# Kernel tuning notes

Hardware: AMD Instinct MI355X
Metric: run time of the kernel (lower is better)

## Reference

```python
import jax, jax.numpy as jnp
import numpy as np

NEG_SLOPE = 0.2

def _leaky(x):
    return jnp.where(x >= 0, x, NEG_SLOPE * x)

def _unigat(X, W, b, ae, av, pair_e, pair_v, num_v, num_e):
    # theta
    Xp = X @ W + b                                                    # [N, d]
    # v2e mean aggregation -> hyperedge features
    deg_e = jax.ops.segment_sum(jnp.ones(pair_e.shape, jnp.float32), pair_e, num_segments=num_e)
    Y = jax.ops.segment_sum(Xp[pair_v], pair_e, num_segments=num_e) / jnp.maximum(deg_e, 1.0)[:, None]  # [E, d]
    # GAT-style attention per incidence pair (edge term + node term), dropout=identity in eval
    s = _leaky((Y @ ae)[pair_e] + (Xp @ av)[pair_v])                  # [P]
    # segment softmax over edges incident to each node
    m = jax.ops.segment_max(s, pair_v, num_segments=num_v)
    ex = jnp.exp(s - m[pair_v])
    den = jax.ops.segment_sum(ex, pair_v, num_segments=num_v)
    alpha = ex / den[pair_v]                                          # [P]
    out = jax.ops.segment_sum(alpha[:, None] * Y[pair_e], pair_v, num_segments=num_v)  # [N, d]
    return jax.nn.elu(out)  # is_last=False everywhere -> ELU (use_bn=False)

def _multi_head(X, W, b, ae, av, pair_e, pair_v, num_v, num_e):
    # W:[H,din,d] b:[H,d] ae/av:[H,d]; concat heads on feature dim
    f = lambda Wh, bh, aeh, avh: _unigat(X, Wh, bh, aeh, avh, pair_e, pair_v, num_v, num_e)
    outs = jax.vmap(f)(W, b, ae, av)                                  # [H, N, d]
    return jnp.transpose(outs, (1, 0, 2)).reshape(X.shape[0], -1)     # [N, H*d]

def setup_inputs() -> dict:
    key = jax.random.key(0)
    ks = jax.random.split(key, 12)
    N, E, P = 100000, 20000, 1600000
    din, dh, H, C = 128, 64, 4, 40
    concat = 2
    inp = {
        "x0": jax.random.normal(ks[0], (N, din), jnp.float32),
        "x1": jax.random.normal(ks[1], (N, din), jnp.float32),
        "W1": jax.random.normal(ks[2], (H, din, dh), jnp.float32) * 0.05,
        "b1": jnp.zeros((H, dh), jnp.float32),
        "ae1": jax.random.normal(ks[3], (H, dh), jnp.float32) * 0.05,
        "av1": jax.random.normal(ks[4], (H, dh), jnp.float32) * 0.05,
        "W2": jax.random.normal(ks[5], (concat * dh * H, C), jnp.float32) * 0.05,
        "b2": jnp.zeros((C,), jnp.float32),
        "ae2": jax.random.normal(ks[6], (C,), jnp.float32) * 0.05,
        "av2": jax.random.normal(ks[7], (C,), jnp.float32) * 0.05,
        "pair_e": jax.random.randint(ks[8], (P,), 0, E, jnp.int32),
        "pair_v": jax.random.randint(ks[9], (P,), 0, N, jnp.int32),
        "num_v": N,
        "num_e": E,
    }
    return inp

def reference(x0, x1, W1, b1, ae1, av1, W2, b2, ae2, av2, pair_e, pair_v, num_v, num_e):
    # dropout layers are identity in eval mode
    h0 = _multi_head(x0, W1, b1, ae1, av1, pair_e, pair_v, num_v, num_e)
    h1 = _multi_head(x1, W1, b1, ae1, av1, pair_e, pair_v, num_v, num_e)
    h = jnp.concatenate([h0, h1], axis=-1)                            # [N, concat*H*dh]
    return _unigat(h, W2, b2, ae2, av2, pair_e, pair_v, num_v, num_e) # [N, C]
```

## Files before the change

kernel.cpp:

```cpp
#include <hip/hip_runtime.h>
#include <cstdint>
#include <cstddef>

static constexpr int DIN = 128;
static constexpr int DH = 64;
static constexpr int NH = 4;
static constexpr int DCAT = 512;
static constexpr int NC = 40;
static constexpr int E_CONST = 20000;
static constexpr int SH_V = 9, SUBD_V = 512;
static constexpr int SH_E = 7, SUBD_E = 128;
static constexpr int ECH = 11, NSUB_E = 10;
static constexpr int VCH = 12, NSUB_V = 25;
static constexpr int CHUNKA = 4096;

typedef unsigned short u16;
typedef __attribute__((ext_vector_type(4))) unsigned short u16x4;
typedef __attribute__((ext_vector_type(8))) unsigned short u16x8;
typedef __attribute__((ext_vector_type(8))) short bf16x8;
typedef __attribute__((ext_vector_type(4))) float f32x4;

static __device__ __forceinline__ float bf2f(u16 u) {
    union { unsigned int i; float f; } x;
    x.i = ((unsigned int)u) << 16;
    return x.f;
}
static __device__ __forceinline__ u16 f2bf(float f) {
    union { float f; unsigned int i; } x;
    x.f = f;
    unsigned int r = x.i + 0x7fffu + ((x.i >> 16) & 1u);
    return (u16)(r >> 16);
}


__global__ void k_hist2(const int* __restrict__ pv, const int* __restrict__ pe,
                        int* __restrict__ btot_v, int* __restrict__ btot_e, int P) {
    __shared__ int cv[256], ce[256];
    int tid = threadIdx.x;
    cv[tid] = 0; ce[tid] = 0;
    __syncthreads();
    int p0 = blockIdx.x * CHUNKA;
    #pragma unroll
    for (int j = 0; j < CHUNKA / 256; ++j) {
        int p = p0 + tid + j * 256;
        if (p < P) {
            atomicAdd(&cv[pv[p] >> SH_V], 1);
            atomicAdd(&ce[pe[p] >> SH_E], 1);
        }
    }
    __syncthreads();
    if (cv[tid]) atomicAdd(&btot_v[tid], cv[tid]);
    if (ce[tid]) atomicAdd(&btot_e[tid], ce[tid]);
}

__global__ void k_scan_small(int* __restrict__ a, int n) {
    __shared__ int wsum[16];
    __shared__ int carry_s;
    int tid = threadIdx.x;
    int lane = tid & 63;
    int w = tid >> 6;
    if (tid == 0) carry_s = 0;
    __syncthreads();
    for (int base = 0; base < n; base += 1024) {
        int i = base + tid;
        int v = (i < n) ? a[i] : 0;
        int x = v;
        #pragma unroll
        for (int off = 1; off < 64; off <<= 1) {
            int t = __shfl_up(x, off);
            if (lane >= off) x += t;
        }
        if (lane == 63) wsum[w] = x;
        __syncthreads();
        int woff = 0;
        for (int k = 0; k < w; ++k) woff += wsum[k];
        int carry = carry_s;
        if (i < n) a[i] = carry + woff + x - v;
        int tot = 0;
        for (int k = 0; k < 16; ++k) tot += wsum[k];
        __syncthreads();
        if (tid == 0) carry_s = carry + tot;
        __syncthreads();
    }
    if (tid == 0) a[n] = carry_s;
}

__global__ void k_scatter2way(const int* __restrict__ pv, const int* __restrict__ pe,
                              const int* __restrict__ bstart_v, const int* __restrict__ bstart_e,
                              int* __restrict__ cur_v, int* __restrict__ cur_e,
                              uint2* __restrict__ sorted_v, uint2* __restrict__ sorted_e, int P) {
    __shared__ int cv[256], ce[256], posv[256], pose[256];
    int tid = threadIdx.x;
    cv[tid] = 0; ce[tid] = 0;
    __syncthreads();
    int p0 = blockIdx.x * CHUNKA;
    int kv[CHUNKA / 256], ke[CHUNKA / 256];
    #pragma unroll
    for (int j = 0; j < CHUNKA / 256; ++j) {
        int p = p0 + tid + j * 256;
        if (p < P) {
            kv[j] = pv[p];
            ke[j] = pe[p];
            atomicAdd(&cv[kv[j] >> SH_V], 1);
            atomicAdd(&ce[ke[j] >> SH_E], 1);
        } else {
            kv[j] = -1;
            ke[j] = -1;
        }
    }
    __syncthreads();
    if (cv[tid]) posv[tid] = bstart_v[tid] + atomicAdd(&cur_v[tid], cv[tid]);
    if (ce[tid]) pose[tid] = bstart_e[tid] + atomicAdd(&cur_e[tid], ce[tid]);
    __syncthreads();
    #pragma unroll
    for (int j = 0; j < CHUNKA / 256; ++j) {
        if (kv[j] >= 0) {
            int iv = atomicAdd(&posv[kv[j] >> SH_V], 1);
            sorted_v[iv] = make_uint2((unsigned)kv[j], (unsigned)ke[j]);
            int ie = atomicAdd(&pose[ke[j] >> SH_E], 1);
            sorted_e[ie] = make_uint2((unsigned)ke[j], (unsigned)kv[j]);
        }
    }
}

template <int SUBD, int SH, int NSUB, int CSH>
__global__ __launch_bounds__(256) void k_build_ord(const uint2* __restrict__ sorted,
                                                   const int* __restrict__ bstart,
                                                   int* __restrict__ start_out,
                                                   int* __restrict__ deg_out,
                                                   int* __restrict__ csr_out, int D) {
    constexpr int NK2 = SUBD * NSUB;
    constexpr int STRIP = (NK2 + 255) / 256;
    __shared__ int cnt[NK2];
    __shared__ int wsum[4];
    int b = blockIdx.x;
    int tid = threadIdx.x;
    int base_key = b << SH;
    int s0 = bstart[b];
    int cntN = bstart[b + 1] - s0;
    for (int k = tid; k < NK2; k += 256) cnt[k] = 0;
    __syncthreads();
    for (int i = tid; i < cntN; i += 256) {
        uint2 pr = sorted[s0 + i];
        int k2 = ((int)pr.x - base_key) * NSUB + ((int)pr.y >> CSH);
        atomicAdd(&cnt[k2], 1);
    }
    __syncthreads();
    int local[STRIP];
    int sum = 0;
    int t0 = tid * STRIP;
    #pragma unroll
    for (int j = 0; j < STRIP; ++j) {
        int idx = t0 + j;
        local[j] = (idx < NK2) ? cnt[idx] : 0;
        sum += local[j];
    }
    int lane = tid & 63, w = tid >> 6;
    int x = sum;
    #pragma unroll
    for (int off = 1; off < 64; off <<= 1) {
        int t = __shfl_up(x, off);
        if (lane >= off) x += t;
    }
    if (lane == 63) wsum[w] = x;
    __syncthreads();
    int woff = 0;
    for (int k = 0; k < w; ++k) woff += wsum[k];
    int run = woff + x - sum;
    __syncthreads();
    #pragma unroll
    for (int j = 0; j < STRIP; ++j) {
        int idx = t0 + j;
        if (idx < NK2) {
            int tmp = local[j];
            cnt[idx] = run;
            run += tmp;
        }
    }
    __syncthreads();
    for (int loc = tid; loc < SUBD; loc += 256) {
        int key = base_key + loc;
        if (key < D) {
            int st = cnt[loc * NSUB];
            int en = (loc == SUBD - 1) ? cntN : cnt[(loc + 1) * NSUB];
            start_out[key] = s0 + st;
            deg_out[key] = en - st;
        }
    }
    __syncthreads();
    for (int i = tid; i < cntN; i += 256) {
        uint2 pr = sorted[s0 + i];
        int k2 = ((int)pr.x - base_key) * NSUB + ((int)pr.y >> CSH);
        int idx = atomicAdd(&cnt[k2], 1);
        csr_out[s0 + idx] = (int)pr.y;
    }
}


__global__ void k_wav(const float* __restrict__ W1, const float* __restrict__ b1,
                      const float* __restrict__ av1, float* __restrict__ wav,
                      float* __restrict__ bav) {
    int h = blockIdx.x;
    int k = threadIdx.x;
    float s = 0.f;
    for (int j = 0; j < DH; ++j) s += W1[(size_t)(h * DIN + k) * DH + j] * av1[h * DH + j];
    wav[h * DIN + k] = s;
    if (k == 0) {
        float t = 0.f;
        for (int j = 0; j < DH; ++j) t += b1[h * DH + j] * av1[h * DH + j];
        bav[h] = t;
    }
}

__global__ void k_build_wcatT(const float* __restrict__ W1, u16* __restrict__ WcatT) {
    int idx = blockIdx.x * 256 + threadIdx.x;
    if (idx >= 256 * DIN) return;
    int c = idx >> 7, k = idx & 127;
    int h = c >> 6, j = c & 63;
    WcatT[c * DIN + k] = f2bf(W1[((size_t)h * DIN + k) * DH + j]);
}

__global__ void k_build_w2T(const float* __restrict__ W2, u16* __restrict__ W2T) {
    int idx = blockIdx.x * 256 + threadIdx.x;
    if (idx >= 48 * DCAT) return;
    int c = idx >> 9, k = idx & 511;
    float v = (c < NC) ? W2[(size_t)k * NC + c] : 0.f;
    W2T[c * DCAT + k] = f2bf(v);
}

__global__ void k_conv(const float* __restrict__ X0, const float* __restrict__ X1,
                       const float* __restrict__ wav, const float* __restrict__ bav,
                       u16* __restrict__ Xbi, float* __restrict__ sv8, int N) {
    int wave = (blockIdx.x * blockDim.x + threadIdx.x) >> 6;
    int lane = threadIdx.x & 63;
    if (wave >= N) return;
    int xz = blockIdx.y;
    const float* X = xz ? X1 : X0;
    float2 a = *(const float2*)(X + (size_t)wave * DIN + lane * 2);
    unsigned int packed = (unsigned int)f2bf(a.x) | ((unsigned int)f2bf(a.y) << 16);
    *(unsigned int*)(Xbi + (size_t)wave * 256 + xz * 128 + lane * 2) = packed;
    float s[NH];
    #pragma unroll
    for (int h = 0; h < NH; ++h) {
        float2 wv = *(const float2*)(wav + h * DIN + lane * 2);
        float t = a.x * wv.x + a.y * wv.y;
        #pragma unroll
        for (int off = 32; off >= 1; off >>= 1) t += __shfl_xor(t, off);
        s[h] = t;
    }
    if (lane == 0) {
        #pragma unroll
        for (int h = 0; h < NH; ++h) sv8[(size_t)wave * 8 + h * 2 + xz] = s[h] + bav[h];
    }
}

__global__ void k_edge_mean1(const u16* __restrict__ Xbi, const int* __restrict__ start_e,
                             const int* __restrict__ deg_e, const int* __restrict__ csr_e_v,
                             u16* __restrict__ Xbar0, u16* __restrict__ Xbar1, int E) {
    int wave = (blockIdx.x * blockDim.x + threadIdx.x) >> 6;
    int lane = threadIdx.x & 63;
    if (wave >= E) return;
    int s = start_e[wave], t = s + deg_e[wave];
    int q = lane >> 4, c = lane & 15;
    float a0[8], a1[8];
    #pragma unroll
    for (int j = 0; j < 8; ++j) { a0[j] = 0.f; a1[j] = 0.f; }
    int i = s + q;
    u16x8 y0A = {0}, y1A = {0}, y0B = {0}, y1B = {0}, y0C = {0}, y1C = {0};
#define EM1_LOAD(Y0, Y1, IDX) { int v_ = csr_e_v[IDX]; \
        const u16* yp_ = Xbi + (size_t)v_ * 256 + c * 8; \
        Y0 = *(const u16x8*)yp_; Y1 = *(const u16x8*)(yp_ + 128); }
#define EM1_CONSUME(Y0, Y1) { \
        _Pragma("unroll") \
        for (int j = 0; j < 8; ++j) { a0[j] += bf2f(Y0[j]); a1[j] += bf2f(Y1[j]); } }
    if (i < t) EM1_LOAD(y0A, y1A, i);
    if (i + 4 < t) EM1_LOAD(y0B, y1B, i + 4);
    if (i + 8 < t) EM1_LOAD(y0C, y1C, i + 8);
    for (; i + 8 < t; i += 12) {
        EM1_CONSUME(y0A, y1A);
        if (i + 12 < t) EM1_LOAD(y0A, y1A, i + 12);
        EM1_CONSUME(y0B, y1B);
        if (i + 16 < t) EM1_LOAD(y0B, y1B, i + 16);
        EM1_CONSUME(y0C, y1C);
        if (i + 20 < t) EM1_LOAD(y0C, y1C, i + 20);
    }
    if (i < t) EM1_CONSUME(y0A, y1A);
    if (i + 4 < t) EM1_CONSUME(y0B, y1B);
#undef EM1_LOAD
#undef EM1_CONSUME
    #pragma unroll
    for (int j = 0; j < 8; ++j) {
        a0[j] += __shfl_xor(a0[j], 16);
        a0[j] += __shfl_xor(a0[j], 32);
        a1[j] += __shfl_xor(a1[j], 16);
        a1[j] += __shfl_xor(a1[j], 32);
    }
    int deg = t - s;
    float inv = 1.f / (float)(deg > 1 ? deg : 1);
    if (q == 0) {
        u16x8 r0, r1;
        #pragma unroll
        for (int j = 0; j < 8; ++j) { r0[j] = f2bf(a0[j] * inv); r1[j] = f2bf(a1[j] * inv); }
        *(u16x8*)(Xbar0 + (size_t)wave * DIN + c * 8) = r0;
        *(u16x8*)(Xbar1 + (size_t)wave * DIN + c * 8) = r1;
    }
}

template <int KDIM, int NTILES, int DOTMODE>
__global__ __launch_bounds__(256) void k_gemm_mfma(const u16* __restrict__ A0,
                                                   const u16* __restrict__ A1, int M,
                                                   const u16* __restrict__ Bt,
                                                   const float* __restrict__ bias,
                                                   u16* __restrict__ out0, u16* __restrict__ out1,
                                                   int ldo, int ncols,
                                                   const float* __restrict__ dvec,
                                                   float* __restrict__ dout) {
    constexpr int LDB = KDIM + 8;
    __shared__ u16 Bs[NTILES * 16 * LDB];
    const u16* A = blockIdx.z ? A1 : A0;
    u16* out = blockIdx.z ? out1 : out0;
    int tid = threadIdx.x;
    int colbase = blockIdx.y * NTILES * 16;
    const u16* Btblk = Bt + (size_t)colbase * KDIM;
    for (int idx = tid * 4; idx < NTILES * 16 * KDIM; idx += 256 * 4) {
        int c = idx / KDIM, k = idx % KDIM;
        *(u16x4*)&Bs[c * LDB + k] = *(const u16x4*)(Btblk + c * KDIM + k);
    }
    __syncthreads();
    int w = tid >> 6, lane = tid & 63;
    int r0 = blockIdx.x * 64 + w * 16;
    int arow = r0 + (lane & 15);
    bool avalid = arow < M;
    const u16* ap = A + (size_t)arow * KDIM + (lane >> 4) * 8;
    f32x4 acc[NTILES];
    #pragma unroll
    for (int nt = 0; nt < NTILES; ++nt) acc[nt] = (f32x4){0.f, 0.f, 0.f, 0.f};
    #pragma unroll
    for (int k0 = 0; k0 < KDIM; k0 += 32) {
        bf16x8 a = (bf16x8)(short)0;
        if (avalid) a = *(const bf16x8*)(ap + k0);
        #pragma unroll
        for (int nt = 0; nt < NTILES; ++nt) {
            bf16x8 b = *(const bf16x8*)&Bs[(nt * 16 + (lane & 15)) * LDB + k0 + (lane >> 4) * 8];
            acc[nt] = __builtin_amdgcn_mfma_f32_16x16x32_bf16(a, b, acc[nt], 0, 0, 0);
        }
    }
    #pragma unroll
    for (int j = 0; j < 4; ++j) {
        int row = r0 + (lane >> 4) * 4 + j;
        float pA = 0.f, pB = 0.f;
        #pragma unroll
        for (int nt = 0; nt < NTILES; ++nt) {
            int col = colbase + nt * 16 + (lane & 15);
            bool cok = col < ncols;
            float val = cok ? acc[nt][j] + bias[col] : 0.f;
            if (DOTMODE == 1) {
                float dv = dvec[col];
                if (nt < NTILES / 2) pA += val * dv; else pB += val * dv;
            } else if (DOTMODE == 2) {
                pA += cok ? val * dvec[col] : 0.f;
            }
            if (row < M && cok) out[(size_t)row * ldo + col] = f2bf(val);
        }
        if (DOTMODE) {
            pA += __shfl_xor(pA, 1);
            pA += __shfl_xor(pA, 2);
            pA += __shfl_xor(pA, 4);
            pA += __shfl_xor(pA, 8);
            if (DOTMODE == 1) {
                pB += __shfl_xor(pB, 1);
                pB += __shfl_xor(pB, 2);
                pB += __shfl_xor(pB, 4);
                pB += __shfl_xor(pB, 8);
            }
            if ((lane & 15) == 0 && row < M) {
                if (DOTMODE == 1) {
                    int hbase = blockIdx.y * 2;
                    int z = blockIdx.z;
                    dout[(size_t)row * 8 + hbase * 2 + z] = pA;
                    dout[(size_t)row * 8 + (hbase + 1) * 2 + z] = pB;
                } else {
                    dout[row] = pA;
                }
            }
        }
    }
}

__global__ void k_node_pass1(const u16* __restrict__ Ycat, const float* __restrict__ se8,
                             const float* __restrict__ sv8, const int* __restrict__ start_v,
                             const int* __restrict__ deg_v, const int* __restrict__ csr_v_e,
                             u16* __restrict__ hbuf, int N) {
    int wave = (blockIdx.x * blockDim.x + threadIdx.x) >> 6;
    int lane = threadIdx.x & 63;
    if (wave >= N) return;
    int p0 = start_v[wave], p1 = p0 + deg_v[wave];
    int g = lane >> 5;
    int c = lane & 31;
    int h = c >> 3;
    u16* orow = hbuf + (size_t)wave * DCAT + c * 8;
    if (p1 == p0) {
        if (g == 0) {
            u16x8 z8 = {0, 0, 0, 0, 0, 0, 0, 0};
            *(u16x8*)orow = z8;
            *(u16x8*)(orow + 256) = z8;
        }
        return;
    }
    float sv0 = sv8[(size_t)wave * 8 + h * 2];
    float sv1 = sv8[(size_t)wave * 8 + h * 2 + 1];
    float den0 = 0.f, den1 = 0.f;
    float a0[8], a1[8];
    #pragma unroll
    for (int j = 0; j < 8; ++j) { a0[j] = 0.f; a1[j] = 0.f; }
    for (int i = p0 + g; i < p1; i += 2) {
        int e = csr_v_e[i];
        float2 s2 = *(const float2*)(se8 + e * 8 + h * 2);
        float x0 = s2.x + sv0;
        float x1 = s2.y + sv1;
        x0 = fmaxf(x0, 0.2f * x0);
        x1 = fmaxf(x1, 0.2f * x1);
        float e0 = __expf(x0);
        float e1 = __expf(x1);
        den0 += e0;
        den1 += e1;
        const u16* yp = Ycat + (size_t)e * 512 + c * 8;
        u16x8 q0 = *(const u16x8*)yp;
        u16x8 q1 = *(const u16x8*)(yp + 256);
        #pragma unroll
        for (int j = 0; j < 8; ++j) { a0[j] += e0 * bf2f(q0[j]); a1[j] += e1 * bf2f(q1[j]); }
    }
    den0 += __shfl_xor(den0, 32);
    den1 += __shfl_xor(den1, 32);
    #pragma unroll
    for (int j = 0; j < 8; ++j) {
        a0[j] += __shfl_xor(a0[j], 32);
        a1[j] += __shfl_xor(a1[j], 32);
    }
    float i0 = 1.f / den0, i1 = 1.f / den1;
    u16x8 r0, r1;
    #pragma unroll
    for (int j = 0; j < 8; ++j) {
        float o0 = a0[j] * i0;
        float o1 = a1[j] * i1;
        o0 = o0 > 0.f ? o0 : __expf(o0) - 1.f;
        o1 = o1 > 0.f ? o1 : __expf(o1) - 1.f;
        r0[j] = f2bf(o0);
        r1[j] = f2bf(o1);
    }
    if (g == 0) {
        *(u16x8*)orow = r0;
        *(u16x8*)(orow + 256) = r1;
    }
}


__global__ void k_edge_mean2(const u16* __restrict__ Xp2b, const int* __restrict__ start_e,
                             const int* __restrict__ deg_ea, const int* __restrict__ csr_e_v,
                             u16* __restrict__ Y2b, const float* __restrict__ ae2,
                             float* __restrict__ se2, int E) {
    int wave = (blockIdx.x * blockDim.x + threadIdx.x) >> 6;
    int lane = threadIdx.x & 63;
    if (wave >= E) return;
    int s = start_e[wave], t = s + deg_ea[wave];
    int g = lane >> 4, c = lane & 15;
    bool act = c < 10;
    float acc[4];
    #pragma unroll
    for (int j = 0; j < 4; ++j) acc[j] = 0.f;
    for (int i = s + g; i < t; i += 4) {
        int v = csr_e_v[i];
        if (act) {
            u16x4 y = *(const u16x4*)(Xp2b + (size_t)v * NC + c * 4);
            acc[0] += bf2f(y.x);
            acc[1] += bf2f(y.y);
            acc[2] += bf2f(y.z);
            acc[3] += bf2f(y.w);
        }
    }
    #pragma unroll
    for (int j = 0; j < 4; ++j) {
        acc[j] += __shfl_xor(acc[j], 16);
        acc[j] += __shfl_xor(acc[j], 32);
    }
    int deg = t - s;
    float inv = 1.f / (float)(deg > 1 ? deg : 1);
    float p = 0.f;
    if (act) {
        float4 ae = *(const float4*)(ae2 + c * 4);
        float y0 = acc[0] * inv, y1 = acc[1] * inv, y2 = acc[2] * inv, y3 = acc[3] * inv;
        p = y0 * ae.x + y1 * ae.y + y2 * ae.z + y3 * ae.w;
        if (g == 0) {
            u16x4 r = {f2bf(y0), f2bf(y1), f2bf(y2), f2bf(y3)};
            *(u16x4*)(Y2b + (size_t)wave * NC + c * 4) = r;
        }
    }
    #pragma unroll
    for (int off = 8; off >= 1; off >>= 1) p += __shfl_xor(p, off);
    if (lane == 0) se2[wave] = p;
}

__global__ void k_node_pass2(const u16* __restrict__ Y2b, const float* __restrict__ se2,
                             const float* __restrict__ sv2, const int* __restrict__ start_v,
                             const int* __restrict__ deg_va, const int* __restrict__ csr_v_e,
                             float* __restrict__ out, int N) {
    int wave = (blockIdx.x * blockDim.x + threadIdx.x) >> 6;
    int lane = threadIdx.x & 63;
    if (wave >= N) return;
    int s = start_v[wave], t = s + deg_va[wave];
    int g = lane >> 4, c = lane & 15;
    bool act = c < 10;
    float* orow = out + (size_t)wave * NC;
    if (t == s) {
        if (g == 0 && act) *(float4*)(orow + c * 4) = make_float4(0.f, 0.f, 0.f, 0.f);
        return;
    }
    float svv = sv2[wave];
    float den = 0.f;
    float acc[4];
    #pragma unroll
    for (int j = 0; j < 4; ++j) acc[j] = 0.f;
    for (int i = s + g; i < t; i += 4) {
        int e = csr_v_e[i];
        float x = se2[e] + svv;
        x = fmaxf(x, 0.2f * x);
        float ex = __expf(x);
        den += ex;
        if (act) {
            u16x4 y = *(const u16x4*)(Y2b + (size_t)e * NC + c * 4);
            acc[0] += ex * bf2f(y.x);
            acc[1] += ex * bf2f(y.y);
            acc[2] += ex * bf2f(y.z);
            acc[3] += ex * bf2f(y.w);
        }
    }
    den += __shfl_xor(den, 16);
    den += __shfl_xor(den, 32);
    #pragma unroll
    for (int j = 0; j < 4; ++j) {
        acc[j] += __shfl_xor(acc[j], 16);
        acc[j] += __shfl_xor(acc[j], 32);
    }
    if (g == 0 && act) {
        float inv = 1.f / den;
        float4 o;
        float* op = &o.x;
        #pragma unroll
        for (int j = 0; j < 4; ++j) {
            float v = acc[j] * inv;
            op[j] = v > 0.f ? v : __expf(v) - 1.f;
        }
        *(float4*)(orow + c * 4) = o;
    }
}

extern "C" void kernel_launch(void* const* d_in, const int* in_sizes, int n_in,
                              void* d_out, int out_size, void* d_ws, size_t ws_size,
                              hipStream_t stream) {
    const float* x0 = (const float*)d_in[0];
    const float* x1 = (const float*)d_in[1];
    const float* W1 = (const float*)d_in[2];
    const float* b1 = (const float*)d_in[3];
    const float* ae1 = (const float*)d_in[4];
    const float* av1 = (const float*)d_in[5];
    const float* W2 = (const float*)d_in[6];
    const float* b2 = (const float*)d_in[7];
    const float* ae2 = (const float*)d_in[8];
    const float* av2 = (const float*)d_in[9];
    const int* pe = (const int*)d_in[10];
    const int* pv = (const int*)d_in[11];

    const int N = in_sizes[0] / DIN;
    const int P = in_sizes[10];
    const int E = E_CONST;
    const int NBKT_V = (N + SUBD_V - 1) / SUBD_V;
    const int NBKT_E = (E + SUBD_E - 1) / SUBD_E;

    char* base = (char*)d_ws;
    auto alloc = [&](size_t bytes) -> void* {
        void* p = (void*)base;
        base += (bytes + 255) & ~(size_t)255;
        return p;
    };
    u16* Xbi = (u16*)alloc((size_t)N * 256 * 2);
    u16* hbuf = (u16*)alloc((size_t)N * DCAT * 2);
    u16* Xbar0 = (u16*)alloc((size_t)E * DIN * 2);
    u16* Xbar1 = (u16*)alloc((size_t)E * DIN * 2);
    u16* Ycat = (u16*)alloc((size_t)E * 512 * 2);
    u16* Xp2b = (u16*)alloc((size_t)N * NC * 2);
    u16* Y2b = (u16*)alloc((size_t)E * NC * 2);
    float* se8 = (float*)alloc((size_t)E * 8 * 4);
    float* se2 = (float*)alloc((size_t)E * 4);
    float* sv8 = (float*)alloc((size_t)N * 8 * 4);
    float* sv2 = (float*)alloc((size_t)N * 4);
    float* wav = (float*)alloc((size_t)NH * DIN * 4);
    float* bav = (float*)alloc((size_t)NH * 4);
    u16* WcatT = (u16*)alloc((size_t)256 * DIN * 2);
    u16* W2T = (u16*)alloc((size_t)48 * DCAT * 2);
    uint2* sorted_v = (uint2*)alloc((size_t)P * 8);
    uint2* sorted_e = (uint2*)alloc((size_t)P * 8);
    int* start_v = (int*)alloc((size_t)N * 4);
    int* deg_v = (int*)alloc((size_t)N * 4);
    int* start_e = (int*)alloc((size_t)E * 4);
    int* deg_e = (int*)alloc((size_t)E * 4);
    int* csr_v_e = (int*)alloc((size_t)P * 4);
    int* csr_e_v = (int*)alloc((size_t)P * 4);
    char* zstart = base;
    int* bstart_v = (int*)alloc((size_t)(NBKT_V + 1) * 4);
    int* bstart_e = (int*)alloc((size_t)(NBKT_E + 1) * 4);
    int* cur_v = (int*)alloc((size_t)256 * 4);
    int* cur_e = (int*)alloc((size_t)256 * 4);
    size_t zbytes = (size_t)(base - zstart);

    if ((size_t)(base - (char*)d_ws) > ws_size) return;

    hipMemsetAsync(zstart, 0, zbytes, stream);

    dim3 b256(256);
    int nA = (P + CHUNKA - 1) / CHUNKA;
    k_hist2<<<nA, b256, 0, stream>>>(pv, pe, bstart_v, bstart_e, P);
    k_scan_small<<<1, 1024, 0, stream>>>(bstart_v, NBKT_V);
    k_scan_small<<<1, 1024, 0, stream>>>(bstart_e, NBKT_E);
    k_scatter2way<<<nA, b256, 0, stream>>>(pv, pe, bstart_v, bstart_e, cur_v, cur_e,
                                           sorted_v, sorted_e, P);
    k_build_ord<SUBD_V, SH_V, NSUB_E, ECH><<<NBKT_V, b256, 0, stream>>>(sorted_v, bstart_v,
                                                                        start_v, deg_v,
                                                                        csr_v_e, N);
    k_build_ord<SUBD_E, SH_E, NSUB_V, VCH><<<NBKT_E, b256, 0, stream>>>(sorted_e, bstart_e,
                                                                        start_e, deg_e,
                                                                        csr_e_v, E);

    k_wav<<<NH, DIN, 0, stream>>>(W1, b1, av1, wav, bav);
    k_build_wcatT<<<(256 * DIN + 255) / 256, b256, 0, stream>>>(W1, WcatT);
    k_build_w2T<<<(48 * DCAT + 255) / 256, b256, 0, stream>>>(W2, W2T);

    int gN4 = (N + 3) / 4;
    int gE4 = (E + 3) / 4;
    dim3 gconv(gN4, 2);
    k_conv<<<gconv, b256, 0, stream>>>(x0, x1, wav, bav, Xbi, sv8, N);

    k_edge_mean1<<<gE4, b256, 0, stream>>>(Xbi, start_e, deg_e, csr_e_v, Xbar0, Xbar1, E);
    dim3 g1((E + 63) / 64, 2, 2);
    k_gemm_mfma<DIN, 8, 1><<<g1, b256, 0, stream>>>(Xbar0, Xbar1, E, WcatT, b1,
                                                    Ycat, Ycat + 256, 512, 256, ae1, se8);
    k_node_pass1<<<gN4, b256, 0, stream>>>(Ycat, se8, sv8, start_v, deg_v, csr_v_e, hbuf, N);

    dim3 g2((N + 63) / 64, 1, 1);
    k_gemm_mfma<DCAT, 3, 2><<<g2, b256, 0, stream>>>(hbuf, hbuf, N, W2T, b2, Xp2b, Xp2b,
                                                     NC, NC, av2, sv2);
    k_edge_mean2<<<gE4, b256, 0, stream>>>(Xp2b, start_e, deg_e, csr_e_v, Y2b, ae2, se2, E);
    k_node_pass2<<<gN4, b256, 0, stream>>>(Y2b, se2, sv2, start_v, deg_v, csr_v_e,
                                           (float*)d_out, N);
}
```

Measured before the change: 666.3 us.

## Split node attention pass per head slice and store scores head-major

The per-head attention scores (se8, sv8) are now stored slice-major, `[slice][row]` instead of `[row][8]`, and the GEMM and conversion kernels write them in that order. k_node_pass1 is restructured so each block handles one of the 8 head/input slices for 32 nodes. Eight lanes per node loop serially over that node's incident edges, replacing one 64-lane wave per node covering every slice. The aim is more independent work, contiguous score lookups per slice, and no cross-half shuffle reductions. The cost is more blocks, and the csr index and edge-range loads are repeated once per slice.

```diff
diff --git a/kernel.cpp b/kernel.cpp
--- a/kernel.cpp
+++ b/kernel.cpp
@@ -250,7 +250,7 @@
     }
     if (lane == 0) {
         #pragma unroll
-        for (int h = 0; h < NH; ++h) sv8[(size_t)wave * 8 + h * 2 + xz] = s[h] + bav[h];
+        for (int h = 0; h < NH; ++h) sv8[(size_t)(xz * 4 + h) * N + wave] = s[h] + bav[h];
     }
 }
 
@@ -377,8 +377,8 @@
                 if (DOTMODE == 1) {
                     int hbase = blockIdx.y * 2;
                     int z = blockIdx.z;
-                    dout[(size_t)row * 8 + hbase * 2 + z] = pA;
-                    dout[(size_t)row * 8 + (hbase + 1) * 2 + z] = pB;
+                    dout[(size_t)(z * 4 + hbase) * M + row] = pA;
+                    dout[(size_t)(z * 4 + hbase + 1) * M + row] = pB;
                 } else {
                     dout[row] = pA;
                 }
@@ -390,68 +390,42 @@
 __global__ void k_node_pass1(const u16* __restrict__ Ycat, const float* __restrict__ se8,
                              const float* __restrict__ sv8, const int* __restrict__ start_v,
                              const int* __restrict__ deg_v, const int* __restrict__ csr_v_e,
-                             u16* __restrict__ hbuf, int N) {
-    int wave = (blockIdx.x * blockDim.x + threadIdx.x) >> 6;
+                             u16* __restrict__ hbuf, int N, int E) {
+    int bid = blockIdx.x;
+    int s = bid & 7;
+    int warp = threadIdx.x >> 6;
     int lane = threadIdx.x & 63;
-    if (wave >= N) return;
-    int p0 = start_v[wave], p1 = p0 + deg_v[wave];
-    int g = lane >> 5;
-    int c = lane & 31;
-    int h = c >> 3;
-    u16* orow = hbuf + (size_t)wave * DCAT + c * 8;
-    if (p1 == p0) {
-        if (g == 0) {
-            u16x8 z8 = {0, 0, 0, 0, 0, 0, 0, 0};
-            *(u16x8*)orow = z8;
-            *(u16x8*)(orow + 256) = z8;
-        }
-        return;
-    }
-    float sv0 = sv8[(size_t)wave * 8 + h * 2];
-    float sv1 = sv8[(size_t)wave * 8 + h * 2 + 1];
-    float den0 = 0.f, den1 = 0.f;
-    float a0[8], a1[8];
-    #pragma unroll
-    for (int j = 0; j < 8; ++j) { a0[j] = 0.f; a1[j] = 0.f; }
-    for (int i = p0 + g; i < p1; i += 2) {
+    int g = lane >> 3, c = lane & 7;
+    int node = (bid >> 3) * 32 + warp * 8 + g;
+    if (node >= N) return;
+    int p0 = start_v[node];
+    int p1 = p0 + deg_v[node];
+    float sv = sv8[(size_t)s * N + node];
+    const float* seS = se8 + (size_t)s * E;
+    const u16* ybase = Ycat + s * 64 + c * 8;
+    float den = 0.f;
+    float acc[8];
+    #pragma unroll
+    for (int j = 0; j < 8; ++j) acc[j] = 0.f;
+    for (int i = p0; i < p1; ++i) {
         int e = csr_v_e[i];
-        float2 s2 = *(const float2*)(se8 + e * 8 + h * 2);
-        float x0 = s2.x + sv0;
-        float x1 = s2.y + sv1;
-        x0 = fmaxf(x0, 0.2f * x0);
-        x1 = fmaxf(x1, 0.2f * x1);
-        float e0 = __expf(x0);
-        float e1 = __expf(x1);
-        den0 += e0;
-        den1 += e1;
-        const u16* yp = Ycat + (size_t)e * 512 + c * 8;
-        u16x8 q0 = *(const u16x8*)yp;
-        u16x8 q1 = *(const u16x8*)(yp + 256);
-        #pragma unroll
-        for (int j = 0; j < 8; ++j) { a0[j] += e0 * bf2f(q0[j]); a1[j] += e1 * bf2f(q1[j]); }
-    }
-    den0 += __shfl_xor(den0, 32);
-    den1 += __shfl_xor(den1, 32);
+        float x = seS[e] + sv;
+        x = fmaxf(x, 0.2f * x);
+        float ex = __expf(x);
+        den += ex;
+        u16x8 y = *(const u16x8*)(ybase + (size_t)e * 512);
+        #pragma unroll
+        for (int j = 0; j < 8; ++j) acc[j] += ex * bf2f(y[j]);
+    }
+    float inv = (p1 > p0) ? 1.f / den : 0.f;
+    u16x8 r;
     #pragma unroll
     for (int j = 0; j < 8; ++j) {
-        a0[j] += __shfl_xor(a0[j], 32);
-        a1[j] += __shfl_xor(a1[j], 32);
-    }
-    float i0 = 1.f / den0, i1 = 1.f / den1;
-    u16x8 r0, r1;
-    #pragma unroll
-    for (int j = 0; j < 8; ++j) {
-        float o0 = a0[j] * i0;
-        float o1 = a1[j] * i1;
-        o0 = o0 > 0.f ? o0 : __expf(o0) - 1.f;
-        o1 = o1 > 0.f ? o1 : __expf(o1) - 1.f;
-        r0[j] = f2bf(o0);
-        r1[j] = f2bf(o1);
-    }
-    if (g == 0) {
-        *(u16x8*)orow = r0;
-        *(u16x8*)(orow + 256) = r1;
-    }
+        float o = acc[j] * inv;
+        o = o > 0.f ? o : __expf(o) - 1.f;
+        r[j] = f2bf(o);
+    }
+    *(u16x8*)(hbuf + (size_t)node * DCAT + s * 64 + c * 8) = r;
 }
 
 
@@ -589,9 +563,9 @@
     u16* Ycat = (u16*)alloc((size_t)E * 512 * 2);
     u16* Xp2b = (u16*)alloc((size_t)N * NC * 2);
     u16* Y2b = (u16*)alloc((size_t)E * NC * 2);
-    float* se8 = (float*)alloc((size_t)E * 8 * 4);
+    float* se8 = (float*)alloc((size_t)8 * E * 4);
     float* se2 = (float*)alloc((size_t)E * 4);
-    float* sv8 = (float*)alloc((size_t)N * 8 * 4);
+    float* sv8 = (float*)alloc((size_t)8 * N * 4);
     float* sv2 = (float*)alloc((size_t)N * 4);
     float* wav = (float*)alloc((size_t)NH * DIN * 4);
     float* bav = (float*)alloc((size_t)NH * 4);
@@ -643,7 +617,9 @@
     dim3 g1((E + 63) / 64, 2, 2);
     k_gemm_mfma<DIN, 8, 1><<<g1, b256, 0, stream>>>(Xbar0, Xbar1, E, WcatT, b1,
                                                     Ycat, Ycat + 256, 512, 256, ae1, se8);
-    k_node_pass1<<<gN4, b256, 0, stream>>>(Ycat, se8, sv8, start_v, deg_v, csr_v_e, hbuf, N);
+    int gnp1 = ((N + 31) / 32) * 8;
+    k_node_pass1<<<gnp1, b256, 0, stream>>>(Ycat, se8, sv8, start_v, deg_v, csr_v_e,
+                                            hbuf, N, E);
 
     dim3 g2((N + 63) / 64, 1, 1);
     k_gemm_mfma<DCAT, 3, 2><<<g2, b256, 0, stream>>>(hbuf, hbuf, N, W2T, b2, Xp2b, Xp2b,
```

Result: faster. 642.5 us (-3.6%).
